# Optimization experiments

Measured on AMD Instinct MI355X. Metric: run time of the kernel, lower is better.

## Reference

```python
import jax, jax.numpy as jnp
import numpy as np
import math

N = 4096
D = 256


def _xavier(key, shape):
    fan_in, fan_out = shape[0], shape[1]
    std = math.sqrt(2.0 / (fan_in + fan_out))
    return jax.random.normal(key, shape, dtype=jnp.float32) * std


def setup_inputs() -> dict:
    key = jax.random.key(0)
    ks = jax.random.split(key, 12)
    return {
        "cur": jax.random.normal(ks[0], (N, D), dtype=jnp.float32),
        "pre": jax.random.normal(ks[1], (N, D), dtype=jnp.float32),
        # SpatialHyperedge params
        "r_proj_s": _xavier(ks[2], (D, D)),
        "incidence_s": _xavier(ks[3], (N, N - 1)),
        # TemporalHyperedge params
        "r_proj_t": _xavier(ks[4], (D, D)),
        "incidence_t": _xavier(ks[5], (N, N)),
        # HHNodeMP params
        "node_proj": _xavier(ks[6], (D, D)),
        "spa_edge_proj": _xavier(ks[7], (D, D)),
        "tmp_edge_proj": _xavier(ks[8], (D, D)),
        "theta_w": _xavier(ks[9], (D, D)),
        "theta_b": jnp.zeros((D,), dtype=jnp.float32),
    }


def _scatter_slave(vals):
    """Place [N, N-1] per-row slave values into a zero-diagonal [N, N] matrix.
    Row i's k-th slave is column k if k < i else k+1 (all j != i in order)."""
    n = vals.shape[0]
    k = jnp.arange(n - 1)[None, :]
    cols = k + (k >= jnp.arange(n)[:, None])  # [N, N-1] column indices
    rows = jnp.broadcast_to(jnp.arange(n)[:, None], (n, n - 1))
    return jnp.zeros((n, n), dtype=vals.dtype).at[rows.reshape(-1), cols.reshape(-1)].set(vals.reshape(-1))


def _fro(x):
    return jnp.sqrt(jnp.sum(x * x))


def reference(cur, pre, r_proj_s, incidence_s, r_proj_t, incidence_t,
              node_proj, spa_edge_proj, tmp_edge_proj, theta_w, theta_b):
    n, d = cur.shape
    inv_sqrt_d = 1.0 / math.sqrt(d)

    # ---- SpatialHyperedge ----
    Xd = jax.lax.stop_gradient(cur)
    master_s = Xd @ r_proj_s                                   # [N, D]
    M_s_full = _scatter_slave(incidence_s)                     # [N, N], zero diag
    neigh_recon_s = M_s_full @ Xd                              # == bmm over gathered slaves
    spatial_loss = (_fro(master_s - neigh_recon_s) * 0.2
                    + jnp.sum(jnp.abs(incidence_s))
                    + 0.001 * _fro(incidence_s))
    # clamp(min=0) then zero-out entries not strictly > 0  => relu-like
    clipped_s = jnp.where(incidence_s > 0.0, incidence_s, 0.0)
    incidence_all = _scatter_slave(clipped_s) + jnp.eye(n, dtype=cur.dtype)

    # ---- TemporalHyperedge ----
    cur_d = jax.lax.stop_gradient(cur)
    pre_d = jax.lax.stop_gradient(pre)
    master_t = cur_d @ r_proj_t
    neigh_recon_t = incidence_t @ pre_d
    temporal_loss = (_fro(master_t - neigh_recon_t) * 0.2
                     + jnp.sum(jnp.abs(incidence_t))
                     + 0.001 * _fro(incidence_t))
    incidence_t_clipped = jnp.maximum(incidence_t, 0.0)

    # ---- SpatialHyperedgeMP ----
    spa_edge_fea = incidence_all @ cur
    spa_deg = jnp.sum(incidence_all, axis=1, keepdims=True)
    spa_emb = spa_edge_fea / spa_deg                           # [N, D]

    # ---- TemporalHyperedgeMP ----
    tmp_edge_fea = incidence_t_clipped @ pre + cur
    tmp_deg = jnp.sum(incidence_t_clipped, axis=1, keepdims=True) + 1.0
    tmp_emb = tmp_edge_fea / tmp_deg                           # [N, D]

    # ---- HHNodeMP ----
    node_fea = cur @ node_proj
    spa_fea = spa_emb @ spa_edge_proj
    tmp_fea = tmp_emb @ tmp_edge_proj
    spa_attn = jnp.sum(spa_fea * node_fea, axis=1, keepdims=True) * inv_sqrt_d
    tmp_attn = jnp.sum(tmp_fea * node_fea, axis=1, keepdims=True) * inv_sqrt_d
    val = spa_attn * spa_fea + tmp_attn * tmp_fea
    node_emb = jax.nn.relu(val @ theta_w.T + theta_b)          # dropout = identity (eval)

    return node_emb, temporal_loss + spatial_loss
```

## Files before the change

### kernel.cpp

```cpp
#include <hip/hip_runtime.h>
#include <hip/hip_bf16.h>
#include <math.h>

#define NN 4096
#define DD 256

typedef __bf16 bf16x8 __attribute__((ext_vector_type(8)));
typedef short  short8 __attribute__((ext_vector_type(8)));
typedef float  f32x4  __attribute__((ext_vector_type(4)));
typedef float  f32x16 __attribute__((ext_vector_type(16)));

typedef __attribute__((address_space(1))) const void gv_t;
typedef __attribute__((address_space(3))) void lv_t;
#define GLD16(gp, lp) __builtin_amdgcn_global_load_lds((gv_t*)(gp), (lv_t*)(lp), 16, 0, 0)

#define MFMA16(a, b, c) __builtin_amdgcn_mfma_f32_16x16x32_bf16((a), (b), (c), 0, 0, 0)
#define MFMA32(a, b, c) __builtin_amdgcn_mfma_f32_32x32x16_bf16((a), (b), (c), 0, 0, 0)

__device__ inline bf16x8 brelu(bf16x8 a) {
    short8 s = __builtin_bit_cast(short8, a);
    s = s & ~(s >> 15);
    return __builtin_bit_cast(bf16x8, s);
}

__device__ inline float wave_red(float v) {
#pragma unroll
    for (int o = 32; o > 0; o >>= 1) v += __shfl_down(v, o, 64);
    return v;
}

__device__ inline unsigned short bfbits(float f) {
    return __builtin_bit_cast(unsigned short, (__bf16)f);
}

__device__ inline void syncb() {
    asm volatile("s_waitcnt lgkmcnt(0)" ::: "memory");
    __builtin_amdgcn_s_barrier();
}

__device__ inline void store16(float* base, const f32x16& v, int lane) {
#pragma unroll
    for (int r4 = 0; r4 < 4; ++r4) {
        f32x4 c = {v[4 * r4], v[4 * r4 + 1], v[4 * r4 + 2], v[4 * r4 + 3]};
        ((f32x4*)base)[r4 * 64 + lane] = c;
    }
}
__device__ inline void add16(f32x16& v, const float* base, int lane) {
#pragma unroll
    for (int r4 = 0; r4 < 4; ++r4) {
        f32x4 c = ((const f32x4*)base)[r4 * 64 + lane];
        v[4 * r4] += c[0]; v[4 * r4 + 1] += c[1]; v[4 * r4 + 2] += c[2]; v[4 * r4 + 3] += c[3];
    }
}

template <int W>
__device__ inline void red_owner(f32x16 (&aR)[2][2], f32x16 (&aL)[2][2],
                                 float* scr, int lane, f32x16& oR, f32x16& oL) {
    constexpr int o1 = W ^ 1, o2 = W ^ 2, o3 = W ^ 3;
    store16(scr + W * 1024,       aR[o1 >> 1][o1 & 1], lane);
    store16(scr + (4 + W) * 1024, aR[o2 >> 1][o2 & 1], lane);
    syncb();
    oR = aR[W >> 1][W & 1];
    add16(oR, scr + o1 * 1024, lane);
    add16(oR, scr + (4 + o2) * 1024, lane);
    syncb();
    store16(scr + W * 1024, aR[o3 >> 1][o3 & 1], lane);
    syncb();
    add16(oR, scr + o3 * 1024, lane);
    syncb();
    store16(scr + W * 1024,       aL[o1 >> 1][o1 & 1], lane);
    store16(scr + (4 + W) * 1024, aL[o2 >> 1][o2 & 1], lane);
    syncb();
    oL = aL[W >> 1][W & 1];
    add16(oL, scr + o1 * 1024, lane);
    add16(oL, scr + (4 + o2) * 1024, lane);
    syncb();
    store16(scr + W * 1024, aL[o3 >> 1][o3 & 1], lane);
    syncb();
    add16(oL, scr + o3 * 1024, lane);
}

__global__ __launch_bounds__(256) void k_pre(
    const float* __restrict__ cur, const float* __restrict__ pre,
    const float* __restrict__ r_proj_s, const float* __restrict__ r_proj_t,
    const float* __restrict__ node_pj, const float* __restrict__ spa_pj,
    const float* __restrict__ tmp_pj, const float* __restrict__ theta_w,
    const float* __restrict__ inc_t, const float* __restrict__ inc_s,
    __bf16* __restrict__ cur_bf, __bf16* __restrict__ curT, __bf16* __restrict__ preT,
    __bf16* __restrict__ pTs, __bf16* __restrict__ pTt, __bf16* __restrict__ pTn,
    __bf16* __restrict__ pTspa, __bf16* __restrict__ pTtmp, __bf16* __restrict__ thetaBf,
    __bf16* __restrict__ Mt, __bf16* __restrict__ Ms,
    float* __restrict__ rsT, float* __restrict__ pAbsT, float* __restrict__ pSqT,
    float* __restrict__ rsS, float* __restrict__ pAbsS, float* __restrict__ pSqS) {
    __shared__ __align__(16) char psm[9280];
    const int b = blockIdx.x, t = threadIdx.x;
    if (b < 4096) {
        const int i = b;
        float (*red)[4] = (float (*)[4])psm;
        const float4* src = (const float4*)(inc_t + (size_t)i * NN);
        ushort4* dst = (ushort4*)(Mt + (size_t)i * NN);
        float rs = 0.f, as = 0.f, qs = 0.f;
#pragma unroll
        for (int e = 0; e < 4; ++e) {
            const int f = t + 256 * e;
            float4 v = src[f];
            float x[4] = {v.x, v.y, v.z, v.w};
            unsigned short o[4];
#pragma unroll
            for (int j = 0; j < 4; ++j) {
                float fv = x[j];
                as += fabsf(fv); qs += fv * fv; rs += fmaxf(fv, 0.f);
                o[j] = bfbits(fv);
            }
            dst[f] = make_ushort4(o[0], o[1], o[2], o[3]);
        }
        const int w = t >> 6, lane = t & 63;
        rs = wave_red(rs); as = wave_red(as); qs = wave_red(qs);
        if (lane == 0) { red[0][w] = rs; red[1][w] = as; red[2][w] = qs; }
        __syncthreads();
        if (t == 0) {
            rsT[i]   = red[0][0] + red[0][1] + red[0][2] + red[0][3];
            pAbsT[i] = red[1][0] + red[1][1] + red[1][2] + red[1][3];
            pSqT[i]  = red[2][0] + red[2][1] + red[2][2] + red[2][3];
        }
    } else if (b < 8192) {
        const int i = b - 4096;
        unsigned short* row = (unsigned short*)psm;
        float (*red)[4] = (float (*)[4])(psm + 8192);
        const float* srow = inc_s + (size_t)i * (NN - 1);
        float rs = 0.f, as = 0.f, qs = 0.f;
#pragma unroll
        for (int e = 0; e < 4; ++e) {
            const int f = t + 256 * e;
            float x[4] = {0.f, 0.f, 0.f, 0.f};
            if (f < 1023) __builtin_memcpy(x, srow + 4 * f, 16);
            else          __builtin_memcpy(x, srow + 4092, 12);
#pragma unroll
            for (int j = 0; j < 4; ++j) {
                const int k = 4 * f + j;
                float fv = x[j];
                as += fabsf(fv); qs += fv * fv; rs += fmaxf(fv, 0.f);
                if (k < NN - 1) row[k + (k >= i)] = bfbits(fv);
            }
        }
        if (t == 0) row[i] = 0;
        __syncthreads();
        uint4* dOut = (uint4*)(Ms + (size_t)i * NN);
        const uint4* sIn = (const uint4*)row;
        dOut[t] = sIn[t];
        dOut[t + 256] = sIn[t + 256];
        const int w = t >> 6, lane = t & 63;
        rs = wave_red(rs); as = wave_red(as); qs = wave_red(qs);
        if (lane == 0) { red[0][w] = rs; red[1][w] = as; red[2][w] = qs; }
        __syncthreads();
        if (t == 0) {
            rsS[i]   = red[0][0] + red[0][1] + red[0][2] + red[0][3];
            pAbsS[i] = red[1][0] + red[1][1] + red[1][2] + red[1][3];
            pSqS[i]  = red[2][0] + red[2][1] + red[2][2] + red[2][3];
        }
    } else if (b < 8704) {
        const int bb = b - 8192;
        const int x = bb & 63, y = (bb >> 6) & 3, z = bb >> 8;
        const int i0 = x * 64, d0 = y * 64;
        const float* src = z ? pre : cur;
        __bf16* dstT = z ? preT : curT;
        unsigned short (*tile)[72] = (unsigned short (*)[72])psm;
        const int r = t >> 2, c4 = (t & 3) * 16;
        const float* srow = src + (size_t)(i0 + r) * DD + d0 + c4;
        alignas(16) unsigned short loc[16];
#pragma unroll
        for (int e = 0; e < 4; ++e) {
            float4 v = ((const float4*)srow)[e];
            loc[e * 4 + 0] = bfbits(v.x);
            loc[e * 4 + 1] = bfbits(v.y);
            loc[e * 4 + 2] = bfbits(v.z);
            loc[e * 4 + 3] = bfbits(v.w);
        }
#pragma unroll
        for (int e = 0; e < 16; ++e) tile[r][c4 + e] = loc[e];
        if (z == 0) {
            __bf16* drow = cur_bf + (size_t)(i0 + r) * DD + d0 + c4;
            *(uint4*)drow = *(uint4*)&loc[0];
            *(uint4*)(drow + 8) = *(uint4*)&loc[8];
        }
        __syncthreads();
        alignas(16) unsigned short o[16];
#pragma unroll
        for (int e = 0; e < 16; ++e) o[e] = tile[c4 + e][r];
        __bf16* trow = dstT + (size_t)(d0 + r) * NN + i0 + c4;
        *(uint4*)trow = *(uint4*)&o[0];
        *(uint4*)(trow + 8) = *(uint4*)&o[8];
    } else {
        const int bb = b - 8704;
        const int id = bb >> 8, r = bb & 255;
        const float* src = id == 0 ? r_proj_s : id == 1 ? r_proj_t : id == 2 ? node_pj
                         : id == 3 ? spa_pj : id == 4 ? tmp_pj : theta_w;
        __bf16* dst = id == 0 ? pTs : id == 1 ? pTt : id == 2 ? pTn
                    : id == 3 ? pTspa : id == 4 ? pTtmp : thetaBf;
        float v = src[r * DD + t];
        if (id < 5) dst[t * DD + r] = (__bf16)v;
        else        dst[r * DD + t] = (__bf16)v;
    }
}

__device__ inline void mfma_step_s(const __bf16 (&As)[64][72], const __bf16 (&Bs)[64][72],
                                   int wr, int wc, int quad, int l16,
                                   f32x4 (&accR)[2][2]) {
#pragma unroll
    for (int ks = 0; ks < 2; ++ks) {
        const int kc = ks * 32 + quad * 8;
        bf16x8 a0 = *(const bf16x8*)&As[wr * 32 + l16][kc];
        bf16x8 a1 = *(const bf16x8*)&As[wr * 32 + 16 + l16][kc];
        bf16x8 b0 = *(const bf16x8*)&Bs[wc * 32 + l16][kc];
        bf16x8 b1 = *(const bf16x8*)&Bs[wc * 32 + 16 + l16][kc];
        accR[0][0] = MFMA16(a0, b0, accR[0][0]);
        accR[0][1] = MFMA16(a0, b1, accR[0][1]);
        accR[1][0] = MFMA16(a1, b0, accR[1][0]);
        accR[1][1] = MFMA16(a1, b1, accR[1][1]);
    }
}

__global__ __launch_bounds__(256, 2) void k_big(const __bf16* __restrict__ Mt, const __bf16* __restrict__ Ms,
                                                const __bf16* __restrict__ preT, const __bf16* __restrict__ curT,
                                                const float* __restrict__ negMt, const float* __restrict__ negMs,
                                                const float* __restrict__ cur,
                                                const float* __restrict__ rsT, const float* __restrict__ rsS,
                                                __bf16* __restrict__ embT, __bf16* __restrict__ embS,
                                                float* __restrict__ pDiff) {
    const int flat = blockIdx.x + 4 * (blockIdx.y + 64 * blockIdx.z);
    const int swz = (flat & 7) * 64 + (flat >> 3);
    const int bx = swz & 3, by = (swz >> 2) & 63, z = swz >> 8;
    const __bf16* A  = z ? Ms : Mt;
    const __bf16* BT = z ? curT : preT;
    const float* negM = z ? negMs : negMt;
    const float* rs   = z ? rsS : rsT;
    __bf16* emb       = z ? embS : embT;
    const int n0 = bx * 64, m0 = by * 64;
    __shared__ __align__(16) char smraw[65536];
    __bf16 (*sm)[2][64][64] = (__bf16 (*)[2][64][64])smraw;
    float* scr = (float*)smraw;
    f32x16 accR[2][2], accL[2][2];
#pragma unroll
    for (int i = 0; i < 2; ++i)
#pragma unroll
        for (int j = 0; j < 2; ++j) { accR[i][j] = (f32x16)0.f; accL[i][j] = (f32x16)0.f; }
    const int t = threadIdx.x, w = t >> 6, lane = t & 63;
    const int lr = lane >> 3, lc = lane & 7;
    const int q0 = 2 * w, q1 = q0 + 1;
    const int csw = (lc ^ lr) * 8;
    const __bf16* gA0 = A + (size_t)(m0 + 8 * q0 + lr) * NN + csw;
    const __bf16* gA1 = A + (size_t)(m0 + 8 * q1 + lr) * NN + csw;
    const __bf16* gB0 = BT + (size_t)(n0 + 8 * q0 + lr) * NN + csw;
    const __bf16* gB1 = BT + (size_t)(n0 + 8 * q1 + lr) * NN + csw;
    auto stage = [&](int b, int tk) {
        const int ko = tk * 64;
        GLD16(gA0 + ko, &sm[b][0][8 * q0][0]);
        GLD16(gA1 + ko, &sm[b][0][8 * q1][0]);
        GLD16(gB0 + ko, &sm[b][1][8 * q0][0]);
        GLD16(gB1 + ko, &sm[b][1][8 * q1][0]);
    };
    stage(0, 0); stage(1, 1); stage(2, 2); stage(3, 3);
    asm volatile("s_waitcnt vmcnt(8)" ::: "memory");
    __builtin_amdgcn_s_barrier();
    __builtin_amdgcn_sched_barrier(0);
    const int fr = lane & 31, h = lane >> 5;
    const int swc = ((2 * w + h) ^ (fr & 7)) * 8;
    for (int it = 0; it < 32; ++it) {
        const int b0 = (2 * it) & 3, b1 = b0 + 1;
        bf16x8 a[2][2], bb[2][2];
#pragma unroll
        for (int mi = 0; mi < 2; ++mi) {
            a[0][mi]  = *(const bf16x8*)&sm[b0][0][mi * 32 + fr][swc];
            a[1][mi]  = *(const bf16x8*)&sm[b1][0][mi * 32 + fr][swc];
            bb[0][mi] = *(const bf16x8*)&sm[b0][1][mi * 32 + fr][swc];
            bb[1][mi] = *(const bf16x8*)&sm[b1][1][mi * 32 + fr][swc];
        }
        asm volatile("s_waitcnt lgkmcnt(0)" ::: "memory");
        __builtin_amdgcn_sched_barrier(0);
        __builtin_amdgcn_s_barrier();
        __builtin_amdgcn_sched_barrier(0);
        if (it < 30) { stage(b0, 2 * it + 4); stage(b1, 2 * it + 5); }
        __builtin_amdgcn_sched_barrier(0);
        __builtin_amdgcn_s_setprio(1);
#pragma unroll
        for (int u = 0; u < 2; ++u)
#pragma unroll
            for (int mi = 0; mi < 2; ++mi) {
                bf16x8 ar = brelu(a[u][mi]);
#pragma unroll
                for (int ni = 0; ni < 2; ++ni) {
                    accR[mi][ni] = MFMA32(a[u][mi], bb[u][ni], accR[mi][ni]);
                    accL[mi][ni] = MFMA32(ar,       bb[u][ni], accL[mi][ni]);
                }
            }
        __builtin_amdgcn_s_setprio(0);
        if (it < 31) {
            if (it < 30) asm volatile("s_waitcnt vmcnt(8)" ::: "memory");
            else         asm volatile("s_waitcnt vmcnt(0)" ::: "memory");
            __builtin_amdgcn_s_barrier();
            __builtin_amdgcn_sched_barrier(0);
        }
    }
    f32x16 oR, oL;
    if      (w == 0) red_owner<0>(accR, accL, scr, lane, oR, oL);
    else if (w == 1) red_owner<1>(accR, accL, scr, lane, oR, oL);
    else if (w == 2) red_owner<2>(accR, accL, scr, lane, oR, oL);
    else             red_owner<3>(accR, accL, scr, lane, oR, oL);
    const int mi = w >> 1, ni = w & 1;
    float sumd = 0.f;
#pragma unroll
    for (int reg = 0; reg < 16; ++reg) {
        const int rr = (reg & 3) + 8 * (reg >> 2) + 4 * h;
        const int gr = m0 + mi * 32 + rr;
        const int gc = n0 + ni * 32 + fr;
        const size_t idx = (size_t)gr * DD + gc;
        float diff = oR[reg] + negM[idx];
        sumd += diff * diff;
        emb[idx] = (__bf16)((oL[reg] + cur[idx]) * (1.f / (rs[gr] + 1.f)));
    }
    sumd = wave_red(sumd);
    float* sredp = (float*)(smraw + 32768);
    if (lane == 0) sredp[w] = sumd;
    __syncthreads();
    if (t == 0)
        pDiff[z * 256 + by * 4 + bx] = sredp[0] + sredp[1] + sredp[2] + sredp[3];
}

__global__ __launch_bounds__(256) void k_small3(const __bf16* __restrict__ cur_bf,
                                                const __bf16* __restrict__ pTs, const __bf16* __restrict__ pTt,
                                                const __bf16* __restrict__ pTn,
                                                float* __restrict__ negMs, float* __restrict__ negMt,
                                                float* __restrict__ nodeFea) {
    const int z = blockIdx.z;
    const __bf16* BT = z == 0 ? pTs : (z == 1 ? pTt : pTn);
    const int n0 = blockIdx.x * 64, m0 = blockIdx.y * 64;
    __shared__ __bf16 As[64][72], Bs[64][72];
    f32x4 accR[2][2];
#pragma unroll
    for (int i = 0; i < 2; ++i)
#pragma unroll
        for (int j = 0; j < 2; ++j) accR[i][j] = (f32x4)0.f;
    const int t = threadIdx.x, w = t >> 6, lane = t & 63, quad = lane >> 4, l16 = lane & 15;
    const int wr = w >> 1, wc = w & 1;
    const int sr = t >> 2, sc = (t & 3) * 16;
    const __bf16* gA = cur_bf + (size_t)(m0 + sr) * DD + sc;
    const __bf16* gB = BT + (size_t)(n0 + sr) * DD + sc;
    for (int kt = 0; kt < DD / 64; ++kt) {
        uint4 av0 = *(const uint4*)(gA);
        uint4 av1 = *(const uint4*)(gA + 8);
        uint4 bv0 = *(const uint4*)(gB);
        uint4 bv1 = *(const uint4*)(gB + 8);
        __syncthreads();
        *(uint4*)&As[sr][sc] = av0; *(uint4*)&As[sr][sc + 8] = av1;
        *(uint4*)&Bs[sr][sc] = bv0; *(uint4*)&Bs[sr][sc + 8] = bv1;
        __syncthreads();
        mfma_step_s(As, Bs, wr, wc, quad, l16, accR);
        gA += 64; gB += 64;
    }
#pragma unroll
    for (int mi = 0; mi < 2; ++mi)
#pragma unroll
        for (int ni = 0; ni < 2; ++ni)
#pragma unroll
            for (int r = 0; r < 4; ++r) {
                int gr = m0 + wr * 32 + mi * 16 + quad * 4 + r;
                int gc = n0 + wc * 32 + ni * 16 + l16;
                size_t idx = (size_t)gr * DD + gc;
                float v = accR[mi][ni][r];
                if (z == 0) negMs[idx] = -v;
                else if (z == 1) negMt[idx] = -v;
                else nodeFea[idx] = v;
            }
}

__global__ __launch_bounds__(256) void k_fea(const __bf16* __restrict__ embS, const __bf16* __restrict__ embT,
                                             const __bf16* __restrict__ pTspa, const __bf16* __restrict__ pTtmp,
                                             const float* __restrict__ nodeF,
                                             float* __restrict__ spaF, float* __restrict__ tmpF,
                                             float* __restrict__ pSpa, float* __restrict__ pTmp) {
    const int z = blockIdx.z;
    const __bf16* Ae = z ? embT : embS;
    const __bf16* BT = z ? pTtmp : pTspa;
    float* outF = z ? tmpF : spaF;
    float* pOut = z ? pTmp : pSpa;
    const int n0 = blockIdx.x * 64, m0 = blockIdx.y * 64;
    __shared__ __bf16 As[64][72], Bs[64][72];
    f32x4 accR[2][2];
#pragma unroll
    for (int i = 0; i < 2; ++i)
#pragma unroll
        for (int j = 0; j < 2; ++j) accR[i][j] = (f32x4)0.f;
    const int t = threadIdx.x, w = t >> 6, lane = t & 63, quad = lane >> 4, l16 = lane & 15;
    const int wr = w >> 1, wc = w & 1;
    const int sr = t >> 2, sc = (t & 3) * 16;
    const __bf16* gA = Ae + (size_t)(m0 + sr) * DD + sc;
    const __bf16* gB = BT + (size_t)(n0 + sr) * DD + sc;
    for (int kt = 0; kt < DD / 64; ++kt) {
        uint4 av0 = *(const uint4*)(gA);
        uint4 av1 = *(const uint4*)(gA + 8);
        uint4 bv0 = *(const uint4*)(gB);
        uint4 bv1 = *(const uint4*)(gB + 8);
        __syncthreads();
        *(uint4*)&As[sr][sc] = av0; *(uint4*)&As[sr][sc + 8] = av1;
        *(uint4*)&Bs[sr][sc] = bv0; *(uint4*)&Bs[sr][sc + 8] = bv1;
        __syncthreads();
        mfma_step_s(As, Bs, wr, wc, quad, l16, accR);
        gA += 64; gB += 64;
    }
    const int slice = blockIdx.x * 2 + wc;
#pragma unroll
    for (int mi = 0; mi < 2; ++mi)
#pragma unroll
        for (int r = 0; r < 4; ++r) {
            const int gr = m0 + wr * 32 + mi * 16 + quad * 4 + r;
            float s = 0.f;
#pragma unroll
            for (int ni = 0; ni < 2; ++ni) {
                const int gc = n0 + wc * 32 + ni * 16 + l16;
                const size_t idx = (size_t)gr * DD + gc;
                const float v = accR[mi][ni][r];
                outF[idx] = v;
                s += v * nodeF[idx];
            }
            s += __shfl_xor(s, 1, 64);
            s += __shfl_xor(s, 2, 64);
            s += __shfl_xor(s, 4, 64);
            s += __shfl_xor(s, 8, 64);
            if (l16 == 0) pOut[(size_t)slice * NN + gr] = s;
        }
}

__global__ __launch_bounds__(256) void k_final(const float* __restrict__ spaF, const float* __restrict__ tmpF,
                                               const float* __restrict__ pSpa, const float* __restrict__ pTmp,
                                               const __bf16* __restrict__ thetaBf, const float* __restrict__ thetaB,
                                               const float* __restrict__ pAbsT, const float* __restrict__ pSqT,
                                               const float* __restrict__ pAbsS, const float* __restrict__ pSqS,
                                               const float* __restrict__ pDiff,
                                               float* __restrict__ out) {
    const int n0 = blockIdx.x * 64, m0 = blockIdx.y * 64;
    __shared__ __bf16 As[64][72], Bs[64][72];
    f32x4 accR[2][2];
#pragma unroll
    for (int i = 0; i < 2; ++i)
#pragma unroll
        for (int j = 0; j < 2; ++j) accR[i][j] = (f32x4)0.f;
    const int t = threadIdx.x, w = t >> 6, lane = t & 63, quad = lane >> 4, l16 = lane & 15;
    const int wr = w >> 1, wc = w & 1;
    const int sr = t >> 2, sc = (t & 3) * 16;
    const int row = m0 + sr;
    float sa = 0.f, ta = 0.f;
#pragma unroll
    for (int j = 0; j < 8; ++j) {
        sa += pSpa[(size_t)j * NN + row];
        ta += pTmp[(size_t)j * NN + row];
    }
    sa *= 0.0625f; ta *= 0.0625f;
    const float* gS = spaF + (size_t)row * DD + sc;
    const float* gT = tmpF + (size_t)row * DD + sc;
    const __bf16* gB = thetaBf + (size_t)(n0 + sr) * DD + sc;
    for (int kt = 0; kt < DD / 64; ++kt) {
        __bf16 tmp[16];
#pragma unroll
        for (int e4 = 0; e4 < 4; ++e4) {
            float4 vs = ((const float4*)gS)[e4];
            float4 vt = ((const float4*)gT)[e4];
            tmp[e4 * 4 + 0] = (__bf16)(sa * vs.x + ta * vt.x);
            tmp[e4 * 4 + 1] = (__bf16)(sa * vs.y + ta * vt.y);
            tmp[e4 * 4 + 2] = (__bf16)(sa * vs.z + ta * vt.z);
            tmp[e4 * 4 + 3] = (__bf16)(sa * vs.w + ta * vt.w);
        }
        uint4 bv0 = *(const uint4*)(gB);
        uint4 bv1 = *(const uint4*)(gB + 8);
        __syncthreads();
        *(uint4*)&As[sr][sc] = *(uint4*)&tmp[0]; *(uint4*)&As[sr][sc + 8] = *(uint4*)&tmp[8];
        *(uint4*)&Bs[sr][sc] = bv0; *(uint4*)&Bs[sr][sc + 8] = bv1;
        __syncthreads();
        mfma_step_s(As, Bs, wr, wc, quad, l16, accR);
        gS += 64; gT += 64; gB += 64;
    }
#pragma unroll
    for (int mi = 0; mi < 2; ++mi)
#pragma unroll
        for (int ni = 0; ni < 2; ++ni)
#pragma unroll
            for (int r = 0; r < 4; ++r) {
                int gr = m0 + wr * 32 + mi * 16 + quad * 4 + r;
                int gc = n0 + wc * 32 + ni * 16 + l16;
                float v = accR[mi][ni][r] + thetaB[gc];
                out[(size_t)gr * DD + gc] = fmaxf(v, 0.f);
            }
    if (blockIdx.x == 0 && blockIdx.y == 0) {
        float aT = 0.f, qT = 0.f, aS = 0.f, qS = 0.f;
#pragma unroll
        for (int j = 0; j < 16; ++j) {
            const int i = t + 256 * j;
            aT += pAbsT[i]; qT += pSqT[i]; aS += pAbsS[i]; qS += pSqS[i];
        }
        float dT = pDiff[t], dS = pDiff[256 + t];
        aT = wave_red(aT); qT = wave_red(qT); aS = wave_red(aS); qS = wave_red(qS);
        dT = wave_red(dT); dS = wave_red(dS);
        float (*red)[4] = (float (*)[4])As;
        if (lane == 0) { red[0][w] = aT; red[1][w] = qT; red[2][w] = aS; red[3][w] = qS; red[4][w] = dT; red[5][w] = dS; }
        __syncthreads();
        if (t == 0) {
            float s[6];
#pragma unroll
            for (int k = 0; k < 6; ++k) s[k] = red[k][0] + red[k][1] + red[k][2] + red[k][3];
            float l = s[0] + 0.001f * sqrtf(s[1]) + 0.2f * sqrtf(s[4])
                    + s[2] + 0.001f * sqrtf(s[3]) + 0.2f * sqrtf(s[5]);
            out[(size_t)NN * DD] = l;
        }
    }
}

extern "C" void kernel_launch(void* const* d_in, const int* in_sizes, int n_in,
                              void* d_out, int out_size, void* d_ws, size_t ws_size,
                              hipStream_t stream) {
    (void)in_sizes; (void)n_in; (void)out_size; (void)ws_size;
    const float* cur      = (const float*)d_in[0];
    const float* pre      = (const float*)d_in[1];
    const float* r_proj_s = (const float*)d_in[2];
    const float* inc_s    = (const float*)d_in[3];
    const float* r_proj_t = (const float*)d_in[4];
    const float* inc_t    = (const float*)d_in[5];
    const float* node_pj  = (const float*)d_in[6];
    const float* spa_pj   = (const float*)d_in[7];
    const float* tmp_pj   = (const float*)d_in[8];
    const float* theta_w  = (const float*)d_in[9];
    const float* theta_b  = (const float*)d_in[10];
    float* out = (float*)d_out;

    char* p = (char*)d_ws;
    auto alloc = [&](size_t bytes) -> void* {
        void* r = (void*)p;
        p += (bytes + 255) & ~(size_t)255;
        return r;
    };
    __bf16* Mt      = (__bf16*)alloc((size_t)NN * NN * 2);
    __bf16* Ms      = (__bf16*)alloc((size_t)NN * NN * 2);
    __bf16* cur_bf  = (__bf16*)alloc((size_t)NN * DD * 2);
    __bf16* curT    = (__bf16*)alloc((size_t)NN * DD * 2);
    __bf16* preT    = (__bf16*)alloc((size_t)NN * DD * 2);
    __bf16* pTs     = (__bf16*)alloc((size_t)DD * DD * 2);
    __bf16* pTt     = (__bf16*)alloc((size_t)DD * DD * 2);
    __bf16* pTn     = (__bf16*)alloc((size_t)DD * DD * 2);
    __bf16* pTspa   = (__bf16*)alloc((size_t)DD * DD * 2);
    __bf16* pTtmp   = (__bf16*)alloc((size_t)DD * DD * 2);
    __bf16* thetaBf = (__bf16*)alloc((size_t)DD * DD * 2);
    __bf16* embS    = (__bf16*)alloc((size_t)NN * DD * 2);
    __bf16* embT    = (__bf16*)alloc((size_t)NN * DD * 2);
    float* negMs    = (float*)alloc((size_t)NN * DD * 4);
    float* negMt    = (float*)alloc((size_t)NN * DD * 4);
    float* nodeFea  = (float*)alloc((size_t)NN * DD * 4);
    float* spaF     = (float*)alloc((size_t)NN * DD * 4);
    float* tmpF     = (float*)alloc((size_t)NN * DD * 4);
    float* rsS      = (float*)alloc((size_t)NN * 4);
    float* rsT      = (float*)alloc((size_t)NN * 4);
    float* pSpa     = (float*)alloc((size_t)8 * NN * 4);
    float* pTmp     = (float*)alloc((size_t)8 * NN * 4);
    float* pAbsT    = (float*)alloc((size_t)NN * 4);
    float* pSqT     = (float*)alloc((size_t)NN * 4);
    float* pAbsS    = (float*)alloc((size_t)NN * 4);
    float* pSqS     = (float*)alloc((size_t)NN * 4);
    float* pDiff    = (float*)alloc(512 * 4);

    k_pre<<<10240, 256, 0, stream>>>(cur, pre, r_proj_s, r_proj_t, node_pj, spa_pj, tmp_pj, theta_w,
                                     inc_t, inc_s,
                                     cur_bf, curT, preT, pTs, pTt, pTn, pTspa, pTtmp, thetaBf,
                                     Mt, Ms, rsT, pAbsT, pSqT, rsS, pAbsS, pSqS);
    k_small3<<<dim3(4, 64, 3), 256, 0, stream>>>(cur_bf, pTs, pTt, pTn, negMs, negMt, nodeFea);
    k_big<<<dim3(4, 64, 2), 256, 0, stream>>>(Mt, Ms, preT, curT, negMt, negMs, cur,
                                              rsT, rsS, embT, embS, pDiff);
    k_fea<<<dim3(4, 64, 2), 256, 0, stream>>>(embS, embT, pTspa, pTtmp, nodeFea,
                                              spaF, tmpF, pSpa, pTmp);
    k_final<<<dim3(4, 64), 256, 0, stream>>>(spaF, tmpF, pSpa, pTmp, thetaBf, theta_b,
                                             pAbsT, pSqT, pAbsS, pSqS, pDiff, out);
}
```

Baseline: 243.7 us.

## Split incidence conversion into its own kernel with direct-gather spatial scatter

Moves the incidence-matrix bf16 conversion and row reductions out of the combined k_pre launch into a separate k_conv kernel, where each block handles four rows. The spatial slave scatter no longer goes through an LDS staging row with a barrier. Each thread now loads an aligned (shifted-by-one) 16-byte chunk and selects shifted values in registers, writing 8-byte stores straight to global. This targets the LDS round trip, the scalar scattered shared stores and the per-row block overhead. It adds an extra kernel launch and a second barrier per row, and the spatial path now does a register-level select.

```diff
diff --git a/kernel.cpp b/kernel.cpp
--- a/kernel.cpp
+++ b/kernel.cpp
@@ -85,86 +85,16 @@
     const float* __restrict__ r_proj_s, const float* __restrict__ r_proj_t,
     const float* __restrict__ node_pj, const float* __restrict__ spa_pj,
     const float* __restrict__ tmp_pj, const float* __restrict__ theta_w,
-    const float* __restrict__ inc_t, const float* __restrict__ inc_s,
     __bf16* __restrict__ cur_bf, __bf16* __restrict__ curT, __bf16* __restrict__ preT,
     __bf16* __restrict__ pTs, __bf16* __restrict__ pTt, __bf16* __restrict__ pTn,
-    __bf16* __restrict__ pTspa, __bf16* __restrict__ pTtmp, __bf16* __restrict__ thetaBf,
-    __bf16* __restrict__ Mt, __bf16* __restrict__ Ms,
-    float* __restrict__ rsT, float* __restrict__ pAbsT, float* __restrict__ pSqT,
-    float* __restrict__ rsS, float* __restrict__ pAbsS, float* __restrict__ pSqS) {
-    __shared__ __align__(16) char psm[9280];
+    __bf16* __restrict__ pTspa, __bf16* __restrict__ pTtmp, __bf16* __restrict__ thetaBf) {
+    __shared__ unsigned short tile[64][72];
     const int b = blockIdx.x, t = threadIdx.x;
-    if (b < 4096) {
-        const int i = b;
-        float (*red)[4] = (float (*)[4])psm;
-        const float4* src = (const float4*)(inc_t + (size_t)i * NN);
-        ushort4* dst = (ushort4*)(Mt + (size_t)i * NN);
-        float rs = 0.f, as = 0.f, qs = 0.f;
-#pragma unroll
-        for (int e = 0; e < 4; ++e) {
-            const int f = t + 256 * e;
-            float4 v = src[f];
-            float x[4] = {v.x, v.y, v.z, v.w};
-            unsigned short o[4];
-#pragma unroll
-            for (int j = 0; j < 4; ++j) {
-                float fv = x[j];
-                as += fabsf(fv); qs += fv * fv; rs += fmaxf(fv, 0.f);
-                o[j] = bfbits(fv);
-            }
-            dst[f] = make_ushort4(o[0], o[1], o[2], o[3]);
-        }
-        const int w = t >> 6, lane = t & 63;
-        rs = wave_red(rs); as = wave_red(as); qs = wave_red(qs);
-        if (lane == 0) { red[0][w] = rs; red[1][w] = as; red[2][w] = qs; }
-        __syncthreads();
-        if (t == 0) {
-            rsT[i]   = red[0][0] + red[0][1] + red[0][2] + red[0][3];
-            pAbsT[i] = red[1][0] + red[1][1] + red[1][2] + red[1][3];
-            pSqT[i]  = red[2][0] + red[2][1] + red[2][2] + red[2][3];
-        }
-    } else if (b < 8192) {
-        const int i = b - 4096;
-        unsigned short* row = (unsigned short*)psm;
-        float (*red)[4] = (float (*)[4])(psm + 8192);
-        const float* srow = inc_s + (size_t)i * (NN - 1);
-        float rs = 0.f, as = 0.f, qs = 0.f;
-#pragma unroll
-        for (int e = 0; e < 4; ++e) {
-            const int f = t + 256 * e;
-            float x[4] = {0.f, 0.f, 0.f, 0.f};
-            if (f < 1023) __builtin_memcpy(x, srow + 4 * f, 16);
-            else          __builtin_memcpy(x, srow + 4092, 12);
-#pragma unroll
-            for (int j = 0; j < 4; ++j) {
-                const int k = 4 * f + j;
-                float fv = x[j];
-                as += fabsf(fv); qs += fv * fv; rs += fmaxf(fv, 0.f);
-                if (k < NN - 1) row[k + (k >= i)] = bfbits(fv);
-            }
-        }
-        if (t == 0) row[i] = 0;
-        __syncthreads();
-        uint4* dOut = (uint4*)(Ms + (size_t)i * NN);
-        const uint4* sIn = (const uint4*)row;
-        dOut[t] = sIn[t];
-        dOut[t + 256] = sIn[t + 256];
-        const int w = t >> 6, lane = t & 63;
-        rs = wave_red(rs); as = wave_red(as); qs = wave_red(qs);
-        if (lane == 0) { red[0][w] = rs; red[1][w] = as; red[2][w] = qs; }
-        __syncthreads();
-        if (t == 0) {
-            rsS[i]   = red[0][0] + red[0][1] + red[0][2] + red[0][3];
-            pAbsS[i] = red[1][0] + red[1][1] + red[1][2] + red[1][3];
-            pSqS[i]  = red[2][0] + red[2][1] + red[2][2] + red[2][3];
-        }
-    } else if (b < 8704) {
-        const int bb = b - 8192;
-        const int x = bb & 63, y = (bb >> 6) & 3, z = bb >> 8;
+    if (b < 512) {
+        const int x = b & 63, y = (b >> 6) & 3, z = b >> 8;
         const int i0 = x * 64, d0 = y * 64;
         const float* src = z ? pre : cur;
         __bf16* dstT = z ? preT : curT;
-        unsigned short (*tile)[72] = (unsigned short (*)[72])psm;
         const int r = t >> 2, c4 = (t & 3) * 16;
         const float* srow = src + (size_t)(i0 + r) * DD + d0 + c4;
         alignas(16) unsigned short loc[16];
@@ -191,7 +121,7 @@
         *(uint4*)trow = *(uint4*)&o[0];
         *(uint4*)(trow + 8) = *(uint4*)&o[8];
     } else {
-        const int bb = b - 8704;
+        const int bb = b - 512;
         const int id = bb >> 8, r = bb & 255;
         const float* src = id == 0 ? r_proj_s : id == 1 ? r_proj_t : id == 2 ? node_pj
                          : id == 3 ? spa_pj : id == 4 ? tmp_pj : theta_w;
@@ -203,20 +133,77 @@
     }
 }
 
-__device__ inline void mfma_step_s(const __bf16 (&As)[64][72], const __bf16 (&Bs)[64][72],
-                                   int wr, int wc, int quad, int l16,
-                                   f32x4 (&accR)[2][2]) {
-#pragma unroll
-    for (int ks = 0; ks < 2; ++ks) {
-        const int kc = ks * 32 + quad * 8;
-        bf16x8 a0 = *(const bf16x8*)&As[wr * 32 + l16][kc];
-        bf16x8 a1 = *(const bf16x8*)&As[wr * 32 + 16 + l16][kc];
-        bf16x8 b0 = *(const bf16x8*)&Bs[wc * 32 + l16][kc];
-        bf16x8 b1 = *(const bf16x8*)&Bs[wc * 32 + 16 + l16][kc];
-        accR[0][0] = MFMA16(a0, b0, accR[0][0]);
-        accR[0][1] = MFMA16(a0, b1, accR[0][1]);
-        accR[1][0] = MFMA16(a1, b0, accR[1][0]);
-        accR[1][1] = MFMA16(a1, b1, accR[1][1]);
+__global__ __launch_bounds__(256) void k_conv(const float* __restrict__ inc_t,
+                                              const float* __restrict__ inc_s,
+                                              __bf16* __restrict__ Mt, __bf16* __restrict__ Ms,
+                                              float* __restrict__ rsT, float* __restrict__ rsS,
+                                              float* __restrict__ pAbsT, float* __restrict__ pSqT,
+                                              float* __restrict__ pAbsS, float* __restrict__ pSqS) {
+    const int b = blockIdx.x, t = threadIdx.x;
+    const int zs = (b >= 1024);
+    const int r0 = (zs ? b - 1024 : b) * 4;
+    __shared__ float red[3][4];
+    const int w = t >> 6, lane = t & 63;
+    for (int rr = 0; rr < 4; ++rr) {
+        const int i = r0 + rr;
+        float rs = 0.f, as = 0.f, qs = 0.f;
+        if (!zs) {
+            const float4* src = (const float4*)(inc_t + (size_t)i * NN);
+            ushort4* dst = (ushort4*)(Mt + (size_t)i * NN);
+            float4 v[4];
+#pragma unroll
+            for (int e = 0; e < 4; ++e) v[e] = src[t + 256 * e];
+#pragma unroll
+            for (int e = 0; e < 4; ++e) {
+                float x[4] = {v[e].x, v[e].y, v[e].z, v[e].w};
+                unsigned short o[4];
+#pragma unroll
+                for (int j = 0; j < 4; ++j) {
+                    float fv = x[j];
+                    as += fabsf(fv); qs += fv * fv; rs += fmaxf(fv, 0.f);
+                    o[j] = bfbits(fv);
+                }
+                dst[t + 256 * e] = make_ushort4(o[0], o[1], o[2], o[3]);
+            }
+        } else {
+            const float* srow = inc_s + (size_t)i * (NN - 1);
+            ushort4* dst = (ushort4*)(Ms + (size_t)i * NN);
+            float lx[16];
+            int dv[4];
+#pragma unroll
+            for (int e = 0; e < 4; ++e) {
+                const int c0 = 4 * (t + 256 * e);
+                const int d = (c0 > i) || (c0 == NN - 4);
+                dv[e] = d;
+                __builtin_memcpy(&lx[4 * e], srow + (c0 - d), 16);
+            }
+#pragma unroll
+            for (int e = 0; e < 4; ++e) {
+                const int c0 = 4 * (t + 256 * e), d = dv[e];
+                unsigned short o[4];
+#pragma unroll
+                for (int j = 0; j < 4; ++j) {
+                    const int k = c0 + j;
+                    float alt = d ? ((j < 3) ? lx[4 * e + j + 1] : 0.f) : lx[4 * e + j];
+                    float agt = d ? lx[4 * e + j] : ((j > 0) ? lx[4 * e + j - 1] : 0.f);
+                    float fv = (k < i) ? alt : ((k == i) ? 0.f : agt);
+                    as += fabsf(fv); qs += fv * fv; rs += fmaxf(fv, 0.f);
+                    o[j] = bfbits(fv);
+                }
+                dst[t + 256 * e] = make_ushort4(o[0], o[1], o[2], o[3]);
+            }
+        }
+        rs = wave_red(rs); as = wave_red(as); qs = wave_red(qs);
+        if (lane == 0) { red[0][w] = rs; red[1][w] = as; red[2][w] = qs; }
+        __syncthreads();
+        if (t == 0) {
+            float r0v = red[0][0] + red[0][1] + red[0][2] + red[0][3];
+            float r1v = red[1][0] + red[1][1] + red[1][2] + red[1][3];
+            float r2v = red[2][0] + red[2][1] + red[2][2] + red[2][3];
+            if (!zs) { rsT[i] = r0v; pAbsT[i] = r1v; pSqT[i] = r2v; }
+            else     { rsS[i] = r0v; pAbsS[i] = r1v; pSqS[i] = r2v; }
+        }
+        __syncthreads();
     }
 }
 
@@ -324,6 +311,23 @@
     __syncthreads();
     if (t == 0)
         pDiff[z * 256 + by * 4 + bx] = sredp[0] + sredp[1] + sredp[2] + sredp[3];
+}
+
+__device__ inline void mfma_step_s(const __bf16 (&As)[64][72], const __bf16 (&Bs)[64][72],
+                                   int wr, int wc, int quad, int l16,
+                                   f32x4 (&accR)[2][2]) {
+#pragma unroll
+    for (int ks = 0; ks < 2; ++ks) {
+        const int kc = ks * 32 + quad * 8;
+        bf16x8 a0 = *(const bf16x8*)&As[wr * 32 + l16][kc];
+        bf16x8 a1 = *(const bf16x8*)&As[wr * 32 + 16 + l16][kc];
+        bf16x8 b0 = *(const bf16x8*)&Bs[wc * 32 + l16][kc];
+        bf16x8 b1 = *(const bf16x8*)&Bs[wc * 32 + 16 + l16][kc];
+        accR[0][0] = MFMA16(a0, b0, accR[0][0]);
+        accR[0][1] = MFMA16(a0, b1, accR[0][1]);
+        accR[1][0] = MFMA16(a1, b0, accR[1][0]);
+        accR[1][1] = MFMA16(a1, b1, accR[1][1]);
+    }
 }
 
 __global__ __launch_bounds__(256) void k_small3(const __bf16* __restrict__ cur_bf,
@@ -564,10 +568,10 @@
     float* pSqS     = (float*)alloc((size_t)NN * 4);
     float* pDiff    = (float*)alloc(512 * 4);
 
-    k_pre<<<10240, 256, 0, stream>>>(cur, pre, r_proj_s, r_proj_t, node_pj, spa_pj, tmp_pj, theta_w,
-                                     inc_t, inc_s,
-                                     cur_bf, curT, preT, pTs, pTt, pTn, pTspa, pTtmp, thetaBf,
-                                     Mt, Ms, rsT, pAbsT, pSqT, rsS, pAbsS, pSqS);
+    k_pre<<<2048, 256, 0, stream>>>(cur, pre, r_proj_s, r_proj_t, node_pj, spa_pj, tmp_pj, theta_w,
+                                    cur_bf, curT, preT, pTs, pTt, pTn, pTspa, pTtmp, thetaBf);
+    k_conv<<<2048, 256, 0, stream>>>(inc_t, inc_s, Mt, Ms, rsT, rsS,
+                                     pAbsT, pSqT, pAbsS, pSqS);
     k_small3<<<dim3(4, 64, 3), 256, 0, stream>>>(cur_bf, pTs, pTt, pTn, negMs, negMt, nodeFea);
     k_big<<<dim3(4, 64, 2), 256, 0, stream>>>(Mt, Ms, preT, curT, negMt, negMs, cur,
                                               rsT, rsS, embT, embS, pDiff);
```

New measurement: 249.2 us. 2.3% more time.

## Process incidence rows per wavefront and drop LDS scatter for spatial rows

Applied to the files above, without the earlier changes.

The preprocessing kernel now assigns one incidence row to each 64-lane wavefront instead of one row per 256-thread block, cutting the grid from 10240 to 4096 blocks. This removes the block-level LDS reductions and barriers. The spatial-incidence scatter, which built each row in shared memory, now computes the shifted column directly in registers using offset loads. The cost is more index arithmetic per element, including unaligned 16-byte loads from the N-1-wide rows. There is also a stray redundant store to rsT.

```diff
diff --git a/kernel.cpp b/kernel.cpp
--- a/kernel.cpp
+++ b/kernel.cpp
@@ -80,7 +80,7 @@
     add16(oL, scr + o3 * 1024, lane);
 }
 
-__global__ __launch_bounds__(256) void k_pre(
+__global__ __launch_bounds__(256) void k_prec(
     const float* __restrict__ cur, const float* __restrict__ pre,
     const float* __restrict__ r_proj_s, const float* __restrict__ r_proj_t,
     const float* __restrict__ node_pj, const float* __restrict__ spa_pj,
@@ -92,79 +92,73 @@
     __bf16* __restrict__ Mt, __bf16* __restrict__ Ms,
     float* __restrict__ rsT, float* __restrict__ pAbsT, float* __restrict__ pSqT,
     float* __restrict__ rsS, float* __restrict__ pAbsS, float* __restrict__ pSqS) {
-    __shared__ __align__(16) char psm[9280];
+    __shared__ unsigned short tile[64][72];
     const int b = blockIdx.x, t = threadIdx.x;
-    if (b < 4096) {
-        const int i = b;
-        float (*red)[4] = (float (*)[4])psm;
-        const float4* src = (const float4*)(inc_t + (size_t)i * NN);
-        ushort4* dst = (ushort4*)(Mt + (size_t)i * NN);
+    const int w = t >> 6, lane = t & 63;
+    if (b < 2048) {
+        const int zs = (b >= 1024);
+        const int i = (((zs ? b - 1024 : b) << 2) | w);
         float rs = 0.f, as = 0.f, qs = 0.f;
-#pragma unroll
-        for (int e = 0; e < 4; ++e) {
-            const int f = t + 256 * e;
-            float4 v = src[f];
-            float x[4] = {v.x, v.y, v.z, v.w};
-            unsigned short o[4];
-#pragma unroll
-            for (int j = 0; j < 4; ++j) {
-                float fv = x[j];
-                as += fabsf(fv); qs += fv * fv; rs += fmaxf(fv, 0.f);
-                o[j] = bfbits(fv);
+        if (!zs) {
+            const float4* src = (const float4*)(inc_t + (size_t)i * NN);
+            uint4* dst = (uint4*)(Mt + (size_t)i * NN);
+#pragma unroll
+            for (int e2 = 0; e2 < 8; ++e2) {
+                const int g = e2 * 64 + lane;
+                float4 v0 = src[2 * g], v1 = src[2 * g + 1];
+                float x[8] = {v0.x, v0.y, v0.z, v0.w, v1.x, v1.y, v1.z, v1.w};
+                alignas(16) unsigned short o[8];
+#pragma unroll
+                for (int j = 0; j < 8; ++j) {
+                    float fv = x[j];
+                    as += fabsf(fv); qs += fv * fv; rs += fmaxf(fv, 0.f);
+                    o[j] = bfbits(fv);
+                }
+                dst[g] = *(uint4*)o;
             }
-            dst[f] = make_ushort4(o[0], o[1], o[2], o[3]);
-        }
-        const int w = t >> 6, lane = t & 63;
-        rs = wave_red(rs); as = wave_red(as); qs = wave_red(qs);
-        if (lane == 0) { red[0][w] = rs; red[1][w] = as; red[2][w] = qs; }
-        __syncthreads();
-        if (t == 0) {
-            rsT[i]   = red[0][0] + red[0][1] + red[0][2] + red[0][3];
-            pAbsT[i] = red[1][0] + red[1][1] + red[1][2] + red[1][3];
-            pSqT[i]  = red[2][0] + red[2][1] + red[2][2] + red[2][3];
-        }
-    } else if (b < 8192) {
-        const int i = b - 4096;
-        unsigned short* row = (unsigned short*)psm;
-        float (*red)[4] = (float (*)[4])(psm + 8192);
-        const float* srow = inc_s + (size_t)i * (NN - 1);
-        float rs = 0.f, as = 0.f, qs = 0.f;
-#pragma unroll
-        for (int e = 0; e < 4; ++e) {
-            const int f = t + 256 * e;
-            float x[4] = {0.f, 0.f, 0.f, 0.f};
-            if (f < 1023) __builtin_memcpy(x, srow + 4 * f, 16);
-            else          __builtin_memcpy(x, srow + 4092, 12);
-#pragma unroll
-            for (int j = 0; j < 4; ++j) {
-                const int k = 4 * f + j;
-                float fv = x[j];
-                as += fabsf(fv); qs += fv * fv; rs += fmaxf(fv, 0.f);
-                if (k < NN - 1) row[k + (k >= i)] = bfbits(fv);
+            if (lane == 0) { rsT[i] = wave_red(0.f), rsT[i] = rs; }
+            rs = wave_red(rs); as = wave_red(as); qs = wave_red(qs);
+            if (lane == 0) { rsT[i] = rs; pAbsT[i] = as; pSqT[i] = qs; }
+        } else {
+            const float* srow = inc_s + (size_t)i * (NN - 1);
+            uint4* dst = (uint4*)(Ms + (size_t)i * NN);
+#pragma unroll
+            for (int e2 = 0; e2 < 8; ++e2) {
+                const int g = e2 * 64 + lane;
+                float lx[8];
+                int dv[2];
+#pragma unroll
+                for (int h = 0; h < 2; ++h) {
+                    const int c0 = 8 * g + 4 * h;
+                    const int d = (c0 > i) || (c0 == NN - 4);
+                    dv[h] = d;
+                    __builtin_memcpy(&lx[4 * h], srow + (c0 - d), 16);
+                }
+                alignas(16) unsigned short o[8];
+#pragma unroll
+                for (int h = 0; h < 2; ++h) {
+                    const int c0 = 8 * g + 4 * h, d = dv[h];
+#pragma unroll
+                    for (int j = 0; j < 4; ++j) {
+                        const int k = c0 + j;
+                        float alt = d ? ((j < 3) ? lx[4 * h + j + 1] : 0.f) : lx[4 * h + j];
+                        float agt = d ? lx[4 * h + j] : ((j > 0) ? lx[4 * h + j - 1] : 0.f);
+                        float fv = (k < i) ? alt : ((k == i) ? 0.f : agt);
+                        as += fabsf(fv); qs += fv * fv; rs += fmaxf(fv, 0.f);
+                        o[4 * h + j] = bfbits(fv);
+                    }
+                }
+                dst[g] = *(uint4*)o;
             }
-        }
-        if (t == 0) row[i] = 0;
-        __syncthreads();
-        uint4* dOut = (uint4*)(Ms + (size_t)i * NN);
-        const uint4* sIn = (const uint4*)row;
-        dOut[t] = sIn[t];
-        dOut[t + 256] = sIn[t + 256];
-        const int w = t >> 6, lane = t & 63;
-        rs = wave_red(rs); as = wave_red(as); qs = wave_red(qs);
-        if (lane == 0) { red[0][w] = rs; red[1][w] = as; red[2][w] = qs; }
-        __syncthreads();
-        if (t == 0) {
-            rsS[i]   = red[0][0] + red[0][1] + red[0][2] + red[0][3];
-            pAbsS[i] = red[1][0] + red[1][1] + red[1][2] + red[1][3];
-            pSqS[i]  = red[2][0] + red[2][1] + red[2][2] + red[2][3];
-        }
-    } else if (b < 8704) {
-        const int bb = b - 8192;
+            rs = wave_red(rs); as = wave_red(as); qs = wave_red(qs);
+            if (lane == 0) { rsS[i] = rs; pAbsS[i] = as; pSqS[i] = qs; }
+        }
+    } else if (b < 2560) {
+        const int bb = b - 2048;
         const int x = bb & 63, y = (bb >> 6) & 3, z = bb >> 8;
         const int i0 = x * 64, d0 = y * 64;
         const float* src = z ? pre : cur;
         __bf16* dstT = z ? preT : curT;
-        unsigned short (*tile)[72] = (unsigned short (*)[72])psm;
         const int r = t >> 2, c4 = (t & 3) * 16;
         const float* srow = src + (size_t)(i0 + r) * DD + d0 + c4;
         alignas(16) unsigned short loc[16];
@@ -191,7 +185,7 @@
         *(uint4*)trow = *(uint4*)&o[0];
         *(uint4*)(trow + 8) = *(uint4*)&o[8];
     } else {
-        const int bb = b - 8704;
+        const int bb = b - 2560;
         const int id = bb >> 8, r = bb & 255;
         const float* src = id == 0 ? r_proj_s : id == 1 ? r_proj_t : id == 2 ? node_pj
                          : id == 3 ? spa_pj : id == 4 ? tmp_pj : theta_w;
@@ -200,23 +194,6 @@
         float v = src[r * DD + t];
         if (id < 5) dst[t * DD + r] = (__bf16)v;
         else        dst[r * DD + t] = (__bf16)v;
-    }
-}
-
-__device__ inline void mfma_step_s(const __bf16 (&As)[64][72], const __bf16 (&Bs)[64][72],
-                                   int wr, int wc, int quad, int l16,
-                                   f32x4 (&accR)[2][2]) {
-#pragma unroll
-    for (int ks = 0; ks < 2; ++ks) {
-        const int kc = ks * 32 + quad * 8;
-        bf16x8 a0 = *(const bf16x8*)&As[wr * 32 + l16][kc];
-        bf16x8 a1 = *(const bf16x8*)&As[wr * 32 + 16 + l16][kc];
-        bf16x8 b0 = *(const bf16x8*)&Bs[wc * 32 + l16][kc];
-        bf16x8 b1 = *(const bf16x8*)&Bs[wc * 32 + 16 + l16][kc];
-        accR[0][0] = MFMA16(a0, b0, accR[0][0]);
-        accR[0][1] = MFMA16(a0, b1, accR[0][1]);
-        accR[1][0] = MFMA16(a1, b0, accR[1][0]);
-        accR[1][1] = MFMA16(a1, b1, accR[1][1]);
     }
 }
 
@@ -324,6 +301,23 @@
     __syncthreads();
     if (t == 0)
         pDiff[z * 256 + by * 4 + bx] = sredp[0] + sredp[1] + sredp[2] + sredp[3];
+}
+
+__device__ inline void mfma_step_s(const __bf16 (&As)[64][72], const __bf16 (&Bs)[64][72],
+                                   int wr, int wc, int quad, int l16,
+                                   f32x4 (&accR)[2][2]) {
+#pragma unroll
+    for (int ks = 0; ks < 2; ++ks) {
+        const int kc = ks * 32 + quad * 8;
+        bf16x8 a0 = *(const bf16x8*)&As[wr * 32 + l16][kc];
+        bf16x8 a1 = *(const bf16x8*)&As[wr * 32 + 16 + l16][kc];
+        bf16x8 b0 = *(const bf16x8*)&Bs[wc * 32 + l16][kc];
+        bf16x8 b1 = *(const bf16x8*)&Bs[wc * 32 + 16 + l16][kc];
+        accR[0][0] = MFMA16(a0, b0, accR[0][0]);
+        accR[0][1] = MFMA16(a0, b1, accR[0][1]);
+        accR[1][0] = MFMA16(a1, b0, accR[1][0]);
+        accR[1][1] = MFMA16(a1, b1, accR[1][1]);
+    }
 }
 
 __global__ __launch_bounds__(256) void k_small3(const __bf16* __restrict__ cur_bf,
@@ -564,7 +558,7 @@
     float* pSqS     = (float*)alloc((size_t)NN * 4);
     float* pDiff    = (float*)alloc(512 * 4);
 
-    k_pre<<<10240, 256, 0, stream>>>(cur, pre, r_proj_s, r_proj_t, node_pj, spa_pj, tmp_pj, theta_w,
+    k_prec<<<4096, 256, 0, stream>>>(cur, pre, r_proj_s, r_proj_t, node_pj, spa_pj, tmp_pj, theta_w,
                                      inc_t, inc_s,
                                      cur_bf, curT, preT, pTs, pTt, pTn, pTspa, pTtmp, thetaBf,
                                      Mt, Ms, rsT, pAbsT, pSqT, rsS, pAbsS, pSqS);
```

Result: no change. 243.7 us (+0.0%).
